# Performance work log

Measured on AMD Instinct MI355X. Metric: run time of the kernel, lower is better.

## Reference

```python
import jax, jax.numpy as jnp
import numpy as np

B, C, H, W = 8, 256, 64, 64
CELLS_PER_IMAGE = 16
N = B * CELLS_PER_IMAGE  # total cells


def setup_inputs() -> dict:
    key = jax.random.key(0)
    k1, k2 = jax.random.split(key)
    feature_maps = jax.random.normal(k1, (B, C, H, W), dtype=jnp.float32)
    # dense-ish boolean cell masks; with 4096 pixels per mask every cell is nonempty
    cell_masks = jax.random.bernoulli(k2, p=0.25, shape=(N, H, W))
    cell_counts = jnp.full((B,), CELLS_PER_IMAGE, dtype=jnp.int32)
    return {"feature_maps": feature_maps, "cell_masks": cell_masks, "cell_counts": cell_counts}


def reference(feature_maps, cell_masks, cell_counts):
    # method='max', positions=False (constructor defaults).
    # Map each cell to its source image: repeat(arange(B), counts) with a
    # static total length so it is jit-compatible.
    n_cells = cell_masks.shape[0]
    batch = feature_maps.shape[0]
    cell_batch = jnp.repeat(jnp.arange(batch), cell_counts, total_repeat_length=n_cells)
    x = feature_maps[cell_batch]  # (N, C, H, W) gathered per cell
    neg_inf = jnp.asarray(-jnp.inf, x.dtype)
    masked = jnp.where(cell_masks[:, None, :, :], x, neg_inf)
    # max over the masked pixels of each cell -> (N, C)
    return jnp.max(masked, axis=(2, 3))
```

## Files before the change

### kernel.cpp

```cpp
#include <hip/hip_runtime.h>
#include <hip/hip_bf16.h>


#define HW    4096
#define BIMG  8
#define CCH   256
#define NCELL 128

__device__ __forceinline__ void cell_range(const int* counts, int b, int& start, int& cnt) {
    start = 0;
    for (int i = 0; i < b; ++i) start += counts[i];
    if (start > NCELL) start = NCELL;
    cnt = counts[b];
    if (b == BIMG - 1 && start + cnt < NCELL) cnt = NCELL - start;
    if (cnt > 16) cnt = 16;
    if (start + cnt > NCELL) cnt = NCELL - start;
    if (cnt < 0) cnt = 0;
}

__global__ __launch_bounds__(256)
void pack_masks(const void* __restrict__ maskv,
                const int* __restrict__ counts,
                unsigned short* __restrict__ packed) {
    const int tid = threadIdx.x;
    const int l   = tid & 63;
    const int idx = blockIdx.x * 256 + tid;
    const int b = idx >> 12;
    const int p = idx & (HW - 1);

    const unsigned* mw0 = (const unsigned*)maskv;
    unsigned ow = mw0[l * 4] | mw0[l * 4 + 1] | mw0[l * 4 + 2] | mw0[l * 4 + 3];
    #pragma unroll
    for (int d = 1; d < 64; d <<= 1) ow |= __shfl_xor(ow, d, 64);
    const unsigned or0 = ow & 0xFFu, or1 = (ow >> 8) & 0xFFu;
    int msize;
    if (or1 == 0)                        msize = 4;
    else if (or0 == 0x80 || or0 == 0x00) msize = 2;
    else                                 msize = 1;

    int start, cnt;
    cell_range(counts, b, start, cnt);

    unsigned w = 0;
    if (msize == 2) {
        const unsigned short* mh = (const unsigned short*)maskv + (size_t)start * HW + p;
        if (cnt == 16) {
            #pragma unroll
            for (int j = 0; j < 16; ++j)
                w |= (mh[(size_t)j * HW] ? 1u : 0u) << j;
        } else {
            for (int j = 0; j < cnt; ++j)
                w |= (mh[(size_t)j * HW] ? 1u : 0u) << j;
        }
    } else if (msize == 4) {
        const unsigned* mw = (const unsigned*)maskv + (size_t)start * HW + p;
        if (cnt == 16) {
            #pragma unroll
            for (int j = 0; j < 16; ++j)
                w |= (mw[(size_t)j * HW] ? 1u : 0u) << j;
        } else {
            for (int j = 0; j < cnt; ++j)
                w |= (mw[(size_t)j * HW] ? 1u : 0u) << j;
        }
    } else {
        const unsigned char* mb = (const unsigned char*)maskv + (size_t)start * HW + p;
        if (cnt == 16) {
            #pragma unroll
            for (int j = 0; j < 16; ++j)
                w |= (mb[(size_t)j * HW] ? 1u : 0u) << j;
        } else {
            for (int j = 0; j < cnt; ++j)
                w |= (mb[(size_t)j * HW] ? 1u : 0u) << j;
        }
    }
    packed[idx] = (unsigned short)w;
}

__global__ __launch_bounds__(256, 4)
void roipool_main(const void* __restrict__ featv,
                  const unsigned short* __restrict__ packed,
                  const int* __restrict__ counts,
                  void* __restrict__ outv) {
    const int c   = blockIdx.x;
    const int b   = blockIdx.y;
    const int tid = threadIdx.x;
    const int l   = tid & 63;
    const int wv  = tid >> 6;
    const float NEG = -__builtin_inff();
    const unsigned NEGI = 0xFF800000u;

    const unsigned* fw_ = (const unsigned*)featv;
    const unsigned w0 = fw_[l];
    const unsigned eb = (w0 >> 8) & 0x7F;
    const unsigned long long bm = __ballot(eb >= 0x3B && eb <= 0x41);
    const int fbf16 = (__popcll(bm) >= 48);

    int start, cnt;
    cell_range(counts, b, start, cnt);

    const int p0 = tid * 16;

    uint4 pa = *(const uint4*)(packed + ((size_t)b << 12) + p0);
    uint4 pb = *(const uint4*)(packed + ((size_t)b << 12) + p0 + 8);
    const unsigned pmw[8] = {pa.x, pa.y, pa.z, pa.w, pb.x, pb.y, pb.z, pb.w};

    unsigned pe[8], po[8];
    if (fbf16) {
        const unsigned short* fp = (const unsigned short*)featv
                                 + (((size_t)(b * CCH + c)) << 12) + p0;
        uint4 f0 = *(const uint4*)(fp);
        uint4 f1 = *(const uint4*)(fp + 8);
        const unsigned w8[8] = {f0.x, f0.y, f0.z, f0.w, f1.x, f1.y, f1.z, f1.w};
        #pragma unroll
        for (int k = 0; k < 8; ++k) {
            pe[k] = w8[k] << 16;
            po[k] = w8[k] & 0xFFFF0000u;
        }
    } else {
        const float* fp = (const float*)featv + (((size_t)(b * CCH + c)) << 12) + p0;
        #pragma unroll
        for (int q = 0; q < 4; ++q) {
            uint4 a = *(const uint4*)(fp + q * 4);
            pe[q * 2]     = a.x; po[q * 2]     = a.y;
            pe[q * 2 + 1] = a.z; po[q * 2 + 1] = a.w;
        }
    }

    float vmax[16];
    #pragma unroll
    for (int j = 0; j < 16; ++j) vmax[j] = NEG;

    #pragma unroll
    for (int k = 0; k < 8; ++k) {
        const unsigned fe = pe[k], fo = po[k];
        const unsigned mw = pmw[k];
        #pragma unroll
        for (int j = 0; j < 16; ++j) {
            unsigned m0 = (unsigned)(((int)(mw << (31 - j))) >> 31);
            unsigned m1 = (unsigned)(((int)(mw << (15 - j))) >> 31);
            float s0 = __uint_as_float((fe & m0) | (NEGI & ~m0));
            float s1 = __uint_as_float((fo & m1) | (NEGI & ~m1));
            vmax[j] = fmaxf(fmaxf(vmax[j], s0), s1);
        }
    }

    #pragma unroll
    for (int d = 1; d < 64; d <<= 1) {
        #pragma unroll
        for (int j = 0; j < 16; ++j)
            vmax[j] = fmaxf(vmax[j], __shfl_xor(vmax[j], d, 64));
    }

    float v = vmax[0];
    #pragma unroll
    for (int j = 1; j < 16; ++j) v = (l == j) ? vmax[j] : v;

    __shared__ float red[4][16];
    if (l < 16) red[wv][l] = v;
    __syncthreads();
    if (tid < 16) {
        float m = fmaxf(fmaxf(red[0][tid], red[1][tid]),
                        fmaxf(red[2][tid], red[3][tid]));
        if (tid < cnt) {
            const size_t oi = (size_t)(start + tid) * CCH + c;
            if (fbf16) ((__hip_bfloat16*)outv)[oi] = __float2bfloat16(m);
            else       ((float*)outv)[oi]          = m;
        }
    }
}

extern "C" void kernel_launch(void* const* d_in, const int* in_sizes, int n_in,
                              void* d_out, int out_size, void* d_ws, size_t ws_size,
                              hipStream_t stream) {
    const void* feat  = d_in[0];
    const void* masks = d_in[1];
    const int* counts = (const int*)d_in[2];
    unsigned short* packed = (unsigned short*)d_ws;

    pack_masks<<<(BIMG * HW) / 256, 256, 0, stream>>>(masks, counts, packed);

    dim3 grid(CCH, BIMG);
    roipool_main<<<grid, 256, 0, stream>>>(feat, packed, counts, d_out);
}
```

Baseline: 88.20 us.

## Use transpose-style butterfly reduction and hoist loads ahead of format detection

Replaces the per-cell 6-step xor shuffle reduction over 16 values with a recursive halving exchange that needs far fewer shuffles. Feature and mask loads are issued before the dtype detection ballot and cell-range computation so that their latency overlaps. Occupancy hint raised to 8 blocks per CU. In pack_masks, 16-bit mask loads are issued speculatively, which wastes bandwidth when the masks are not 16-bit.

```diff
diff --git a/kernel.cpp b/kernel.cpp
--- a/kernel.cpp
+++ b/kernel.cpp
@@ -29,7 +29,16 @@
     const int p = idx & (HW - 1);
 
     const unsigned* mw0 = (const unsigned*)maskv;
-    unsigned ow = mw0[l * 4] | mw0[l * 4 + 1] | mw0[l * 4 + 2] | mw0[l * 4 + 3];
+    const unsigned o0 = mw0[l * 4], o1 = mw0[l * 4 + 1],
+                   o2 = mw0[l * 4 + 2], o3 = mw0[l * 4 + 3];
+    const unsigned short* mh = (const unsigned short*)maskv + ((size_t)b * 16) * HW + p;
+    unsigned short sv[16];
+    #pragma unroll
+    for (int j = 0; j < 16; ++j) sv[j] = mh[(size_t)j * HW];
+    int start, cnt;
+    cell_range(counts, b, start, cnt);
+
+    unsigned ow = o0 | o1 | o2 | o3;
     #pragma unroll
     for (int d = 1; d < 64; d <<= 1) ow |= __shfl_xor(ow, d, 64);
     const unsigned or0 = ow & 0xFFu, or1 = (ow >> 8) & 0xFFu;
@@ -38,45 +47,24 @@
     else if (or0 == 0x80 || or0 == 0x00) msize = 2;
     else                                 msize = 1;
 
-    int start, cnt;
-    cell_range(counts, b, start, cnt);
-
     unsigned w = 0;
-    if (msize == 2) {
-        const unsigned short* mh = (const unsigned short*)maskv + (size_t)start * HW + p;
-        if (cnt == 16) {
-            #pragma unroll
-            for (int j = 0; j < 16; ++j)
-                w |= (mh[(size_t)j * HW] ? 1u : 0u) << j;
-        } else {
-            for (int j = 0; j < cnt; ++j)
-                w |= (mh[(size_t)j * HW] ? 1u : 0u) << j;
-        }
+    if (msize == 2 && start == b * 16 && cnt == 16) {
+        #pragma unroll
+        for (int j = 0; j < 16; ++j) w |= (sv[j] ? 1u : 0u) << j;
+    } else if (msize == 2) {
+        const unsigned short* m2 = (const unsigned short*)maskv + (size_t)start * HW + p;
+        for (int j = 0; j < cnt; ++j) w |= (m2[(size_t)j * HW] ? 1u : 0u) << j;
     } else if (msize == 4) {
-        const unsigned* mw = (const unsigned*)maskv + (size_t)start * HW + p;
-        if (cnt == 16) {
-            #pragma unroll
-            for (int j = 0; j < 16; ++j)
-                w |= (mw[(size_t)j * HW] ? 1u : 0u) << j;
-        } else {
-            for (int j = 0; j < cnt; ++j)
-                w |= (mw[(size_t)j * HW] ? 1u : 0u) << j;
-        }
+        const unsigned* m4 = (const unsigned*)maskv + (size_t)start * HW + p;
+        for (int j = 0; j < cnt; ++j) w |= (m4[(size_t)j * HW] ? 1u : 0u) << j;
     } else {
-        const unsigned char* mb = (const unsigned char*)maskv + (size_t)start * HW + p;
-        if (cnt == 16) {
-            #pragma unroll
-            for (int j = 0; j < 16; ++j)
-                w |= (mb[(size_t)j * HW] ? 1u : 0u) << j;
-        } else {
-            for (int j = 0; j < cnt; ++j)
-                w |= (mb[(size_t)j * HW] ? 1u : 0u) << j;
-        }
+        const unsigned char* m1 = (const unsigned char*)maskv + (size_t)start * HW + p;
+        for (int j = 0; j < cnt; ++j) w |= (m1[(size_t)j * HW] ? 1u : 0u) << j;
     }
     packed[idx] = (unsigned short)w;
 }
 
-__global__ __launch_bounds__(256, 4)
+__global__ __launch_bounds__(256, 8)
 void roipool_main(const void* __restrict__ featv,
                   const unsigned short* __restrict__ packed,
                   const int* __restrict__ counts,
@@ -89,27 +77,26 @@
     const float NEG = -__builtin_inff();
     const unsigned NEGI = 0xFF800000u;
 
-    const unsigned* fw_ = (const unsigned*)featv;
-    const unsigned w0 = fw_[l];
+    const int p0 = tid * 16;
+
+    const unsigned short* fp16 = (const unsigned short*)featv
+                               + (((size_t)(b * CCH + c)) << 12) + p0;
+    uint4 f0 = *(const uint4*)(fp16);
+    uint4 f1 = *(const uint4*)(fp16 + 8);
+    uint4 pa = *(const uint4*)(packed + ((size_t)b << 12) + p0);
+    uint4 pb = *(const uint4*)(packed + ((size_t)b << 12) + p0 + 8);
+    const unsigned w0 = ((const unsigned*)featv)[l];
+    int start, cnt;
+    cell_range(counts, b, start, cnt);
+
     const unsigned eb = (w0 >> 8) & 0x7F;
     const unsigned long long bm = __ballot(eb >= 0x3B && eb <= 0x41);
     const int fbf16 = (__popcll(bm) >= 48);
 
-    int start, cnt;
-    cell_range(counts, b, start, cnt);
-
-    const int p0 = tid * 16;
-
-    uint4 pa = *(const uint4*)(packed + ((size_t)b << 12) + p0);
-    uint4 pb = *(const uint4*)(packed + ((size_t)b << 12) + p0 + 8);
     const unsigned pmw[8] = {pa.x, pa.y, pa.z, pa.w, pb.x, pb.y, pb.z, pb.w};
 
     unsigned pe[8], po[8];
     if (fbf16) {
-        const unsigned short* fp = (const unsigned short*)featv
-                                 + (((size_t)(b * CCH + c)) << 12) + p0;
-        uint4 f0 = *(const uint4*)(fp);
-        uint4 f1 = *(const uint4*)(fp + 8);
         const unsigned w8[8] = {f0.x, f0.y, f0.z, f0.w, f1.x, f1.y, f1.z, f1.w};
         #pragma unroll
         for (int k = 0; k < 8; ++k) {
@@ -144,19 +131,48 @@
         }
     }
 
-    #pragma unroll
-    for (int d = 1; d < 64; d <<= 1) {
-        #pragma unroll
-        for (int j = 0; j < 16; ++j)
-            vmax[j] = fmaxf(vmax[j], __shfl_xor(vmax[j], d, 64));
-    }
-
-    float v = vmax[0];
-    #pragma unroll
-    for (int j = 1; j < 16; ++j) v = (l == j) ? vmax[j] : v;
+    float v8[8];
+    {
+        const bool s = (l & 1);
+        #pragma unroll
+        for (int j = 0; j < 8; ++j) {
+            float snd = s ? vmax[2*j]   : vmax[2*j+1];
+            float mne = s ? vmax[2*j+1] : vmax[2*j];
+            v8[j] = fmaxf(mne, __shfl_xor(snd, 1, 64));
+        }
+    }
+    float v4[4];
+    {
+        const bool s = (l >> 1) & 1;
+        #pragma unroll
+        for (int j = 0; j < 4; ++j) {
+            float snd = s ? v8[2*j]   : v8[2*j+1];
+            float mne = s ? v8[2*j+1] : v8[2*j];
+            v4[j] = fmaxf(mne, __shfl_xor(snd, 2, 64));
+        }
+    }
+    float v2[2];
+    {
+        const bool s = (l >> 2) & 1;
+        #pragma unroll
+        for (int j = 0; j < 2; ++j) {
+            float snd = s ? v4[2*j]   : v4[2*j+1];
+            float mne = s ? v4[2*j+1] : v4[2*j];
+            v2[j] = fmaxf(mne, __shfl_xor(snd, 4, 64));
+        }
+    }
+    float v1;
+    {
+        const bool s = (l >> 3) & 1;
+        float snd = s ? v2[0] : v2[1];
+        float mne = s ? v2[1] : v2[0];
+        v1 = fmaxf(mne, __shfl_xor(snd, 8, 64));
+    }
+    v1 = fmaxf(v1, __shfl_xor(v1, 16, 64));
+    v1 = fmaxf(v1, __shfl_xor(v1, 32, 64));
 
     __shared__ float red[4][16];
-    if (l < 16) red[wv][l] = v;
+    if (l < 16) red[wv][l] = v1;
     __syncthreads();
     if (tid < 16) {
         float m = fmaxf(fmaxf(red[0][tid], red[1][tid]),
```

After: 89.81 us. Within noise of the previous version (+1.8%).
